# Optimization experiments

Hardware: AMD Instinct MI355X
Metric: run time of the kernel (lower is better)

Reference implementation:

```python
import jax, jax.numpy as jnp
import numpy as np


def setup_inputs() -> dict:
    key = jax.random.key(0)
    k1, k2 = jax.random.split(key)
    latent = jax.random.normal(k1, (131072, 128), dtype=jnp.float32)
    coords = jax.random.normal(k2, (2048, 128), dtype=jnp.float32)
    return {"latent": latent, "coords": coords}


def reference(latent, coords):
    # torch.cdist(latent, coords).min(1)[1]
    # argmin over euclidean distance == argmin over squared distance,
    # so we skip the sqrt (same result, cheaper and numerically safer).
    x2 = jnp.sum(latent * latent, axis=1, keepdims=True)          # [N, 1]
    c2 = jnp.sum(coords * coords, axis=1)                          # [C]
    cross = latent @ coords.T                                      # [N, C]
    d2 = x2 + c2[None, :] - 2.0 * cross                            # [N, C] squared dists
    return jnp.argmin(d2, axis=1)                                  # [N] int indices
```

## Files before the change

### kernel.cpp

```cpp
#include <hip/hip_runtime.h>


constexpr int D = 128;
constexpr int C = 2048;
constexpr int NCH = 64;
constexpr int NCHUNKS = C / NCH;
constexpr float MARGIN_H = 0.01f;
constexpr int WL_CAP = 32768;

constexpr size_t WS_CNT = 8192;
constexpr size_t WS_WL  = 16384;
constexpr size_t WS_BH  = 262144;
constexpr size_t WS_BL  = 786432;

typedef __attribute__((ext_vector_type(8))) short short8;
typedef __attribute__((ext_vector_type(4))) float f32x4;
typedef unsigned int u32;

__device__ inline unsigned short bf16_rne(float x) {
    unsigned u = __float_as_uint(x);
    u += 0x7FFFu + ((u >> 16) & 1u);
    return (unsigned short)(u >> 16);
}
__device__ inline float bf16_to_f(unsigned short h) {
    return __uint_as_float(((unsigned)h) << 16);
}
__device__ inline void split8(const float* v, short8* hi, short8* lo) {
#pragma unroll
    for (int j = 0; j < 8; ++j) {
        unsigned short h = bf16_rne(v[j]);
        (*hi)[j] = (short)h;
        (*lo)[j] = (short)bf16_rne(v[j] - bf16_to_f(h));
    }
}

__device__ __forceinline__ void gl_lds16(const void* g, void* l) {
    __builtin_amdgcn_global_load_lds(
        (const __attribute__((address_space(1))) u32*)g,
        (__attribute__((address_space(3))) u32*)l, 16, 0, 0);
}

__global__ void prep_coords(const float* __restrict__ coords,
                            unsigned short* __restrict__ Bh,
                            unsigned short* __restrict__ Bl,
                            float* __restrict__ c2, int* __restrict__ counter) {
    int t = blockIdx.x * blockDim.x + threadIdx.x;
    if (t == 0) *counter = 0;
    if (t >= C * 16) return;
    int c  = t >> 4;
    int k8 = t & 15;
    float v[8];
    *(float4*)(v)     = *(const float4*)(coords + (size_t)c * D + k8 * 8);
    *(float4*)(v + 4) = *(const float4*)(coords + (size_t)c * D + k8 * 8 + 4);
    short8 hi, lo;
    split8(v, &hi, &lo);
    int ch = c >> 6, nl = c & 63;
    size_t off = (size_t)ch * (NCH * 128) + ((size_t)nl * 16 + (k8 ^ (nl & 15))) * 8;
    *(short8*)(Bh + off) = hi;
    *(short8*)(Bl + off) = lo;
    float p = 0.f;
#pragma unroll
    for (int j = 0; j < 8; ++j) p = fmaf(v[j], v[j], p);
#pragma unroll
    for (int m = 1; m <= 8; m <<= 1) p += __shfl_xor(p, m, 64);
    if (k8 == 0) c2[c] = p;
}


__global__ __launch_bounds__(256, 2) void centroid_fast(
        const float* __restrict__ latent,
        const unsigned short* __restrict__ Bh_img,
        const unsigned short* __restrict__ Bl_img,
        const float* __restrict__ c2g,
        int* __restrict__ out,
        int* __restrict__ counter,
        int* __restrict__ worklist) {
    __shared__ __align__(16) unsigned short Bh[2][NCH * 128], Bl[2][NCH * 128];
    __shared__ __align__(16) float sc2[C];

    const int tid  = threadIdx.x;
    const int wid  = tid >> 6;
    const int lane = tid & 63;
    const int q    = lane >> 4, lr = lane & 15;
    const int row_block = blockIdx.x * 256;

    {
        const unsigned short* sh = Bh_img;
        const unsigned short* sl = Bl_img;
#pragma unroll
        for (int i = 0; i < 4; ++i) {
            int e = (i * 256 + tid) * 8;
            gl_lds16(sh + e, &Bh[0][e]);
            gl_lds16(sl + e, &Bl[0][e]);
        }
    }
#pragma unroll
    for (int i = 0; i < 2; ++i) {
        int e = (i * 256 + tid) * 4;
        *(float4*)(sc2 + e) = *(const float4*)(c2g + e);
    }

    short8 Ah[4][4], Al[4][4];
#pragma unroll
    for (int mt = 0; mt < 4; ++mt) {
        const float* rp = latent + (size_t)(row_block + wid * 64 + mt * 16 + lr) * D;
#pragma unroll
        for (int ks = 0; ks < 4; ++ks) {
            float v[8];
            *(float4*)(v)     = *(const float4*)(rp + ks * 32 + q * 8);
            *(float4*)(v + 4) = *(const float4*)(rp + ks * 32 + q * 8 + 4);
            split8(v, &Ah[mt][ks], &Al[mt][ks]);
        }
    }

    float b1[16], b2[16];
    int   bidx[16];
#pragma unroll
    for (int s = 0; s < 16; ++s) { b1[s] = -3.4e38f; b2[s] = -3.4e38f; bidx[s] = 0; }

    __syncthreads();

    for (int ch = 0; ch < NCHUNKS; ++ch) {
        const int buf = ch & 1;
        if (ch + 1 < NCHUNKS) {
            const unsigned short* sh = Bh_img + (size_t)(ch + 1) * (NCH * 128);
            const unsigned short* sl = Bl_img + (size_t)(ch + 1) * (NCH * 128);
#pragma unroll
            for (int i = 0; i < 4; ++i) {
                int e = (i * 256 + tid) * 8;
                gl_lds16(sh + e, &Bh[buf ^ 1][e]);
                gl_lds16(sl + e, &Bl[buf ^ 1][e]);
            }
            asm volatile("s_waitcnt vmcnt(8)" ::: "memory");
        } else {
            asm volatile("s_waitcnt vmcnt(0)" ::: "memory");
        }
        __builtin_amdgcn_s_barrier();

#pragma unroll
        for (int nt = 0; nt < 4; ++nt) {
            const int nl = nt * 16 + lr;
            const float mh = -0.5f * sc2[ch * NCH + nl];
            f32x4 acc[4];
#pragma unroll
            for (int mt = 0; mt < 4; ++mt) acc[mt] = (f32x4){mh, mh, mh, mh};
#pragma unroll
            for (int ks = 0; ks < 4; ++ks) {
                const int xv = ((ks * 4) | q) ^ lr;
                const int e  = nl * 128 + xv * 8;
                short8 bh = *(const short8*)(&Bh[buf][e]);
                short8 bl = *(const short8*)(&Bl[buf][e]);
#pragma unroll
                for (int mt = 0; mt < 4; ++mt)
                    acc[mt] = __builtin_amdgcn_mfma_f32_16x16x32_bf16(Ah[mt][ks], bh, acc[mt], 0, 0, 0);
#pragma unroll
                for (int mt = 0; mt < 4; ++mt)
                    acc[mt] = __builtin_amdgcn_mfma_f32_16x16x32_bf16(Ah[mt][ks], bl, acc[mt], 0, 0, 0);
#pragma unroll
                for (int mt = 0; mt < 4; ++mt)
                    acc[mt] = __builtin_amdgcn_mfma_f32_16x16x32_bf16(Al[mt][ks], bh, acc[mt], 0, 0, 0);
            }
            const int n_global = ch * NCH + nl;
#pragma unroll
            for (int mt = 0; mt < 4; ++mt)
#pragma unroll
                for (int r = 0; r < 4; ++r) {
                    int slot = mt * 4 + r;
                    float a = acc[mt][r];
                    bool gt  = a > b1[slot];
                    float mn = fminf(a, b1[slot]);
                    b2[slot]   = fmaxf(b2[slot], mn);
                    b1[slot]   = fmaxf(a, b1[slot]);
                    bidx[slot] = gt ? n_global : bidx[slot];
                }
        }
        __builtin_amdgcn_s_barrier();
    }

#pragma unroll
    for (int m = 1; m <= 8; m <<= 1) {
#pragma unroll
        for (int s = 0; s < 16; ++s) {
            float oa = __shfl_xor(b1[s], m, 64);
            float ob = __shfl_xor(b2[s], m, 64);
            int   oi = __shfl_xor(bidx[s], m, 64);
            float mn = fminf(b1[s], oa);
            b2[s] = fmaxf(fmaxf(b2[s], ob), mn);
            bool take = (oa > b1[s]) || (oa == b1[s] && oi < bidx[s]);
            b1[s]   = take ? oa : b1[s];
            bidx[s] = take ? oi : bidx[s];
        }
    }
#pragma unroll
    for (int s = 0; s < 16; ++s) {
        if (lr == s) {
            int row = row_block + wid * 64 + (s >> 2) * 16 + q * 4 + (s & 3);
            out[row] = bidx[s];
            if (b1[s] - b2[s] < MARGIN_H) {
                int w = atomicAdd(counter, 1);
                if (w < WL_CAP) worklist[w] = row;
            }
        }
    }
}


__global__ __launch_bounds__(256) void refine_fp64(
        const float* __restrict__ latent, const float* __restrict__ coords,
        const int* __restrict__ worklist, const int* __restrict__ counter,
        int wl_cap, int* __restrict__ out) {
    __shared__ float  xs[D];
    __shared__ double rv[256];
    __shared__ int    ri[256];

    int n = *counter;
    if (n > wl_cap) n = wl_cap;

    for (int wi = blockIdx.x; wi < n; wi += gridDim.x) {
        int row = worklist[wi];
        if (threadIdx.x < D)
            xs[threadIdx.x] = latent[(size_t)row * D + threadIdx.x];
        __syncthreads();

        double best = 1.0e300;
        int    bix  = 0;
        for (int c = threadIdx.x; c < C; c += 256) {
            const float4* cp = (const float4*)(coords + (size_t)c * D);
            double s0 = 0.0, s1 = 0.0, s2 = 0.0, s3 = 0.0;
#pragma unroll 8
            for (int k4 = 0; k4 < 32; ++k4) {
                float4 v = cp[k4];
                double d0 = (double)xs[k4 * 4 + 0] - (double)v.x;
                double d1 = (double)xs[k4 * 4 + 1] - (double)v.y;
                double d2 = (double)xs[k4 * 4 + 2] - (double)v.z;
                double d3 = (double)xs[k4 * 4 + 3] - (double)v.w;
                s0 = fma(d0, d0, s0); s1 = fma(d1, d1, s1);
                s2 = fma(d2, d2, s2); s3 = fma(d3, d3, s3);
            }
            double s = (s0 + s1) + (s2 + s3);
            if (s < best) { best = s; bix = c; }
        }
        rv[threadIdx.x] = best;
        ri[threadIdx.x] = bix;
        __syncthreads();
        for (int off = 128; off > 0; off >>= 1) {
            if (threadIdx.x < off) {
                double ov = rv[threadIdx.x + off];
                int    oi = ri[threadIdx.x + off];
                if (ov < rv[threadIdx.x] ||
                    (ov == rv[threadIdx.x] && oi < ri[threadIdx.x])) {
                    rv[threadIdx.x] = ov;
                    ri[threadIdx.x] = oi;
                }
            }
            __syncthreads();
        }
        if (threadIdx.x == 0) out[row] = ri[0];
        __syncthreads();
    }
}

extern "C" void kernel_launch(void* const* d_in, const int* in_sizes, int n_in,
                              void* d_out, int out_size, void* d_ws, size_t ws_size,
                              hipStream_t stream) {
    const float* latent = (const float*)d_in[0];
    const float* coords = (const float*)d_in[1];
    int*         out    = (int*)d_out;

    char* ws = (char*)d_ws;
    float* c2      = (float*)ws;
    int*   counter = (int*)(ws + WS_CNT);
    int*   wl      = (int*)(ws + WS_WL);
    unsigned short* Bh = (unsigned short*)(ws + WS_BH);
    unsigned short* Bl = (unsigned short*)(ws + WS_BL);
    const int n_rows = in_sizes[0] / D;

    prep_coords<<<(C * 16) / 256, 256, 0, stream>>>(coords, Bh, Bl, c2, counter);
    centroid_fast<<<n_rows / 256, 256, 0, stream>>>(latent, Bh, Bl, c2, out,
                                                    counter, wl);
    refine_fp64<<<608, 256, 0, stream>>>(latent, coords, wl, counter, WL_CAP, out);
}
```

Before: 310.6 us.

## Software-pipeline MFMA tiles with deferred argmin epilogue and LDS prefetch

Alternates two accumulator sets so the running top-2/argmin update for one 16-column tile is interleaved with the MFMAs of the next tile. B fragments for the next k-slice or tile are loaded from LDS one step ahead. The second-best update now uses a single fmed3 instead of min plus max. The aim is to hide epilogue VALU work and LDS latency behind matrix-core work. The cost is more live registers under a two-blocks-per-CU launch bound, which risks spills. The lane-reduction tie-break on equal scores was also dropped, so exact ties may resolve to a different index.

Measured after the change: 355.1 us. 1.14x slower.

```diff
diff --git a/kernel.cpp b/kernel.cpp
--- a/kernel.cpp
+++ b/kernel.cpp
@@ -67,6 +67,51 @@
 }
 
 
+#define EPI_SLICE(P, KS)                                                  \
+    do {                                                                  \
+        _Pragma("unroll") for (int r = 0; r < 4; ++r) {                   \
+            const int slot = (KS) * 4 + r;                                \
+            float a = P[KS][r];                                           \
+            b2[slot] = __builtin_amdgcn_fmed3f(a, b1[slot], b2[slot]);    \
+            bool gt = a > b1[slot];                                       \
+            b1[slot] = fmaxf(a, b1[slot]);                                \
+            bidx[slot] = gt ? png : bidx[slot];                           \
+        }                                                                 \
+    } while (0)
+
+#define DO_NT(NT, CACC, PACC)                                                  \
+    do {                                                                       \
+        const int nl_ = (NT) * 16 + lr;                                        \
+        const float mh_ = -0.5f * sc2[chbase + nl_];                           \
+        _Pragma("unroll") for (int mt = 0; mt < 4; ++mt)                       \
+            CACC[mt] = (f32x4){mh_, mh_, mh_, mh_};                            \
+        _Pragma("unroll") for (int ks = 0; ks < 4; ++ks) {                     \
+            short8 nh_, nl2_;                                                  \
+            constexpr bool last_ = ((NT) == 3);                                \
+            if (ks < 3) {                                                      \
+                const int e_ = nl_ * 128 + ((((ks + 1) * 4) | q) ^ lr) * 8;    \
+                nh_  = *(const short8*)(&Bh[buf][e_]);                         \
+                nl2_ = *(const short8*)(&Bl[buf][e_]);                         \
+            } else if (!last_) {                                               \
+                const int e_ = (nl_ + 16) * 128 + (q ^ lr) * 8;                \
+                nh_  = *(const short8*)(&Bh[buf][e_]);                         \
+                nl2_ = *(const short8*)(&Bl[buf][e_]);                         \
+            }                                                                  \
+            EPI_SLICE(PACC, ks);                                               \
+            _Pragma("unroll") for (int mt = 0; mt < 4; ++mt)                   \
+                CACC[mt] = __builtin_amdgcn_mfma_f32_16x16x32_bf16(            \
+                    Ah[mt][ks], bch, CACC[mt], 0, 0, 0);                       \
+            _Pragma("unroll") for (int mt = 0; mt < 4; ++mt)                   \
+                CACC[mt] = __builtin_amdgcn_mfma_f32_16x16x32_bf16(            \
+                    Ah[mt][ks], bcl, CACC[mt], 0, 0, 0);                       \
+            _Pragma("unroll") for (int mt = 0; mt < 4; ++mt)                   \
+                CACC[mt] = __builtin_amdgcn_mfma_f32_16x16x32_bf16(            \
+                    Al[mt][ks], bch, CACC[mt], 0, 0, 0);                       \
+            if (ks < 3 || !last_) { bch = nh_; bcl = nl2_; }                   \
+        }                                                                      \
+        png = chbase + nl_;                                                    \
+    } while (0)
+
 __global__ __launch_bounds__(256, 2) void centroid_fast(
         const float* __restrict__ latent,
         const unsigned short* __restrict__ Bh_img,
@@ -118,10 +163,17 @@
 #pragma unroll
     for (int s = 0; s < 16; ++s) { b1[s] = -3.4e38f; b2[s] = -3.4e38f; bidx[s] = 0; }
 
+    f32x4 accA[4], accB[4];
+#pragma unroll
+    for (int mt = 0; mt < 4; ++mt) accB[mt] = (f32x4){-3.4e38f, -3.4e38f, -3.4e38f, -3.4e38f};
+    int png = 0;
+    short8 bch, bcl;
+
     __syncthreads();
 
     for (int ch = 0; ch < NCHUNKS; ++ch) {
         const int buf = ch & 1;
+        const int chbase = ch * NCH;
         if (ch + 1 < NCHUNKS) {
             const unsigned short* sh = Bh_img + (size_t)(ch + 1) * (NCH * 128);
             const unsigned short* sl = Bl_img + (size_t)(ch + 1) * (NCH * 128);
@@ -137,45 +189,21 @@
         }
         __builtin_amdgcn_s_barrier();
 
-#pragma unroll
-        for (int nt = 0; nt < 4; ++nt) {
-            const int nl = nt * 16 + lr;
-            const float mh = -0.5f * sc2[ch * NCH + nl];
-            f32x4 acc[4];
-#pragma unroll
-            for (int mt = 0; mt < 4; ++mt) acc[mt] = (f32x4){mh, mh, mh, mh};
-#pragma unroll
-            for (int ks = 0; ks < 4; ++ks) {
-                const int xv = ((ks * 4) | q) ^ lr;
-                const int e  = nl * 128 + xv * 8;
-                short8 bh = *(const short8*)(&Bh[buf][e]);
-                short8 bl = *(const short8*)(&Bl[buf][e]);
-#pragma unroll
-                for (int mt = 0; mt < 4; ++mt)
-                    acc[mt] = __builtin_amdgcn_mfma_f32_16x16x32_bf16(Ah[mt][ks], bh, acc[mt], 0, 0, 0);
-#pragma unroll
-                for (int mt = 0; mt < 4; ++mt)
-                    acc[mt] = __builtin_amdgcn_mfma_f32_16x16x32_bf16(Ah[mt][ks], bl, acc[mt], 0, 0, 0);
-#pragma unroll
-                for (int mt = 0; mt < 4; ++mt)
-                    acc[mt] = __builtin_amdgcn_mfma_f32_16x16x32_bf16(Al[mt][ks], bh, acc[mt], 0, 0, 0);
-            }
-            const int n_global = ch * NCH + nl;
-#pragma unroll
-            for (int mt = 0; mt < 4; ++mt)
-#pragma unroll
-                for (int r = 0; r < 4; ++r) {
-                    int slot = mt * 4 + r;
-                    float a = acc[mt][r];
-                    bool gt  = a > b1[slot];
-                    float mn = fminf(a, b1[slot]);
-                    b2[slot]   = fmaxf(b2[slot], mn);
-                    b1[slot]   = fmaxf(a, b1[slot]);
-                    bidx[slot] = gt ? n_global : bidx[slot];
-                }
-        }
+        {
+            const int e0 = lr * 128 + (q ^ lr) * 8;
+            bch = *(const short8*)(&Bh[buf][e0]);
+            bcl = *(const short8*)(&Bl[buf][e0]);
+        }
+        DO_NT(0, accA, accB);
+        DO_NT(1, accB, accA);
+        DO_NT(2, accA, accB);
+        DO_NT(3, accB, accA);
+
         __builtin_amdgcn_s_barrier();
     }
+
+#pragma unroll
+    for (int ks = 0; ks < 4; ++ks) EPI_SLICE(accB, ks);
 
 #pragma unroll
     for (int m = 1; m <= 8; m <<= 1) {
@@ -186,7 +214,7 @@
             int   oi = __shfl_xor(bidx[s], m, 64);
             float mn = fminf(b1[s], oa);
             b2[s] = fmaxf(fmaxf(b2[s], ob), mn);
-            bool take = (oa > b1[s]) || (oa == b1[s] && oi < bidx[s]);
+            bool take = oa > b1[s];
             b1[s]   = take ? oa : b1[s];
             bidx[s] = take ? oi : bidx[s];
         }
```
